# Kernel tuning notes

Measured on AMD Instinct MI355X. Metric: run time of the kernel, lower is better.

The kernel has to match this reference:

```python
import jax, jax.numpy as jnp
import numpy as np

N, E, U, R = 50000, 400000, 32, 32
CUTOFF = 5.0


def _xavier(key, shape):
    fan_out, fan_in = shape
    lim = (6.0 / (fan_in + fan_out)) ** 0.5
    return jax.random.uniform(key, shape, jnp.float32, -lim, lim)


def setup_inputs() -> dict:
    key = jax.random.key(0)
    ks = jax.random.split(key, 13)
    X = jax.random.normal(ks[0], (N, 3, 3, U), jnp.float32)
    edge_index = jax.random.randint(ks[1], (2, E), 0, N)
    edge_weight = jax.random.uniform(ks[2], (E,), jnp.float32)
    edge_attr = jax.random.normal(ks[3], (E, R), jnp.float32)
    W1 = _xavier(ks[4], (U, R)); b1 = jnp.zeros((U,), jnp.float32)
    W2 = _xavier(ks[5], (2 * U, U)); b2 = jnp.zeros((2 * U,), jnp.float32)
    W3 = _xavier(ks[6], (3 * U, 2 * U)); b3 = jnp.zeros((3 * U,), jnp.float32)
    Wt = jnp.stack([_xavier(ks[7 + i], (U, U)) for i in range(6)])  # 6 bias-free tensor linears
    return dict(X=X, edge_index=edge_index, edge_weight=edge_weight, edge_attr=edge_attr,
                W1=W1, b1=b1, W2=W2, b2=b2, W3=W3, b3=b3, Wt=Wt)


def _decompose(T):
    # T: (n, 3, 3, u) -> scalar (full eye*trace/3), skew-symmetric, traceless symmetric parts
    Tt = jnp.swapaxes(T, 1, 2)
    trace = jnp.einsum('niiu->nu', T)
    eye = jnp.eye(3, dtype=T.dtype)[None, :, :, None]
    I = (trace / 3.0)[:, None, None, :] * eye
    A = 0.5 * (T - Tt)
    S = 0.5 * (T + Tt) - I
    return I, A, S


def _lin(T, W):
    # torch nn.Linear (no bias): y = x @ W.T over the trailing units axis
    return jnp.einsum('nijk,mk->nijm', T, W)


def reference(X, edge_index, edge_weight, edge_attr, W1, b1, W2, b2, W3, b3, Wt):
    num_nodes = X.shape[0]
    u = X.shape[-1]
    # cosine cutoff
    Cc = jnp.where(edge_weight < CUTOFF,
                   0.5 * (jnp.cos(edge_weight * jnp.pi / CUTOFF) + 1.0), 0.0)
    # scalar edge MLP
    ea = jax.nn.silu(edge_attr @ W1.T + b1)
    ea = jax.nn.silu(ea @ W2.T + b2)
    ea = jax.nn.silu(ea @ W3.T + b3)
    ea = (ea * Cc[:, None]).reshape(-1, u, 3)  # (E, units, 3)
    # normalize node tensors
    normX = jnp.sum(X ** 2, axis=(1, 2)) + 1.0  # (n, u)
    Xn = X / normX[:, None, None, :]
    # decompose + per-component linears
    I, A, S = _decompose(Xn)
    I = _lin(I, Wt[0]); A = _lin(A, Wt[1]); S = _lin(S, Wt[2])
    Y = I + A + S
    # message passing: gather at dst, weight, scatter-add back to dst
    dst = edge_index[1]
    eaI = ea[..., 0][:, None, None, :]
    eaA = ea[..., 1][:, None, None, :]
    eaS = ea[..., 2][:, None, None, :]
    Im = jax.ops.segment_sum(I[dst] * eaI, dst, num_segments=num_nodes)
    Am = jax.ops.segment_sum(A[dst] * eaA, dst, num_segments=num_nodes)
    Sm = jax.ops.segment_sum(S[dst] * eaS, dst, num_segments=num_nodes)
    msg = Im + Am + Sm
    # O(3) tensor product: Y @ msg + msg @ Y (per node, per unit)
    M = jnp.einsum('nijk,njlk->nilk', Y, msg) + jnp.einsum('nijk,njlk->nilk', msg, Y)
    I, A, S = _decompose(M)
    Xc = I + A + S
    normp1 = (jnp.sum(Xc ** 2, axis=(1, 2)) + 1.0)[:, None, None, :]
    I, A, S = I / normp1, A / normp1, S / normp1
    I = _lin(I, Wt[3]); A = _lin(A, Wt[4]); S = _lin(S, Wt[5])
    dX = I + A + S
    return Xn + dX + jnp.einsum('nijk,njlk->nilk', dX, dX)
```

## Files before the change

kernel.cpp:

```cpp
#include <hip/hip_runtime.h>
#include <math.h>


typedef _Float16 h2    __attribute__((ext_vector_type(2)));
typedef __fp16   p2    __attribute__((ext_vector_type(2)));
typedef _Float16 f16x8 __attribute__((ext_vector_type(8)));
typedef float    f32x4 __attribute__((ext_vector_type(4)));

union U8 { unsigned u[4]; uint4 q; f16x8 v; };
union C4 { float4 f; f32x4 v; };

__device__ __forceinline__ h2 as_h2(unsigned u){ union{unsigned x; h2 h;} c; c.x=u; return c.h; }
__device__ __forceinline__ unsigned h2bits(h2 h){ union{h2 h; unsigned x;} c; c.h=h; return c.x; }

__device__ __forceinline__ float dot2(h2 a, h2 b, float c){
#if __has_builtin(__builtin_amdgcn_fdot2)
    return __builtin_amdgcn_fdot2(a, b, c, false);
#else
    return c + (float)a.x*(float)b.x + (float)a.y*(float)b.y;
#endif
}

__device__ __forceinline__ h2 pk(float a, float b){
#if __has_builtin(__builtin_amdgcn_cvt_pkrtz)
    union { p2 p; h2 h; } c;
    c.p = __builtin_amdgcn_cvt_pkrtz(a, b);
    return c.h;
#else
    h2 r; r.x=(_Float16)a; r.y=(_Float16)b; return r;
#endif
}

__device__ __forceinline__ unsigned pk_rtn(float a, float b){
    union { h2 h; unsigned x; } c;
    c.h.x = (_Float16)a; c.h.y = (_Float16)b;
    return c.x;
}

__device__ __forceinline__ float fast_silu(float x){
    return x * __builtin_amdgcn_rcpf(1.0f + __expf(-x));
}

__global__ __launch_bounds__(256) void prep_kernel(
    const float* __restrict__ Wt,
    const float* __restrict__ W1, const float* __restrict__ b1,
    const float* __restrict__ W2, const float* __restrict__ b2,
    const float* __restrict__ W3, const float* __restrict__ b3,
    unsigned* __restrict__ whn, float* __restrict__ ball, unsigned* __restrict__ wfrag)
{
    int i = blockIdx.x * 256 + threadIdx.x;
    if (i < 4096) {
        int call = i >> 11, r = i & 2047, kp = r >> 7, rem = r & 127;
        int u = rem >> 2, c = rem & 3;
        unsigned val = 0;
        if (c < 3) {
            const float* W = Wt + (size_t)(3*call + c)*1024 + u*32 + 2*kp;
            val = pk_rtn(W[0], W[1]);
        }
        whn[i] = val;
    }
    if (i < 192) {
        float v;
        if (i < 32)      v = b1[i];
        else if (i < 96) v = b2[i-32];
        else {
            int o = i - 96;
            v = b3[(o & 31)*3 + (o >> 5)];
        }
        ball[i] = v;
    }
    if (i < 4608) {
        int f = i >> 8, l = (i >> 2) & 63, wi = i & 3;
        int row = l & 15, qq = l >> 4;
        int kb = 8*qq + 2*wi;
        float v0, v1;
        if (f < 2) {
            int m = 16*f + row;
            v0 = W1[m*32 + kb]; v1 = W1[m*32 + kb + 1];
        } else if (f < 6) {
            int m = 16*(f-2) + row;
            v0 = W2[m*32 + kb]; v1 = W2[m*32 + kb + 1];
        } else {
            int idx = f - 6, mt = idx >> 1, kh = idx & 1;
            int mp = 16*mt + row;
            int om = (mp & 31)*3 + (mp >> 5);
            int k  = 32*kh + kb;
            v0 = W3[om*64 + k]; v1 = W3[om*64 + k + 1];
        }
        wfrag[i] = pk_rtn(v0, v1);
    }
}

__global__ __launch_bounds__(256) void hist_kernel(
    const int* __restrict__ edge_index, int* __restrict__ cnt, int nE)
{
    int e = blockIdx.x * 256 + threadIdx.x;
    if (e < nE) atomicAdd(&cnt[edge_index[nE + e]], 1);
}

__global__ __launch_bounds__(1024) void scanA_kernel(
    const int* __restrict__ cnt, int* __restrict__ rowptr,
    int* __restrict__ csum, int nN)
{
    __shared__ int wsum[16];
    __shared__ int wpre[16];
    int tid = threadIdx.x, lane = tid & 63, wid = tid >> 6;
    int i = blockIdx.x * 1024 + tid;
    int orig = (i < nN) ? cnt[i] : 0;
    int v = orig;
    #pragma unroll
    for (int d = 1; d < 64; d <<= 1) { int o = __shfl_up(v, d); if (lane >= d) v += o; }
    if (lane == 63) wsum[wid] = v;
    __syncthreads();
    if (wid == 0) {
        int s = (lane < 16) ? wsum[lane] : 0;
        #pragma unroll
        for (int d = 1; d < 16; d <<= 1) { int o = __shfl_up(s, d); if (lane >= d) s += o; }
        if (lane < 16) wpre[lane] = s;
    }
    __syncthreads();
    int badd = wid ? wpre[wid - 1] : 0;
    if (i < nN) rowptr[i] = badd + v - orig;
    if (tid == 1023) csum[blockIdx.x] = badd + v;
}

__global__ __launch_bounds__(64) void scanB_kernel(
    int* __restrict__ csum, int* __restrict__ rowptr, int nChunks, int nN)
{
    int lane = threadIdx.x;
    int orig = (lane < nChunks) ? csum[lane] : 0;
    int s = orig;
    #pragma unroll
    for (int d = 1; d < 64; d <<= 1) { int o = __shfl_up(s, d); if (lane >= d) s += o; }
    if (lane < nChunks) csum[lane] = s - orig;
    if (lane == 63) rowptr[nN] = s;
}

__global__ __launch_bounds__(1024) void scanC_kernel(
    const int* __restrict__ csum, int* __restrict__ rowptr, int nN)
{
    int i = blockIdx.x * 1024 + threadIdx.x;
    if (i < nN) rowptr[i] += csum[i >> 10];
}

__global__ __launch_bounds__(256, 4) void edge_mfma_kernel(
    const float* __restrict__ edge_attr,
    const float* __restrict__ edge_weight,
    const int* __restrict__ edge_index,
    const int* __restrict__ rowptr,
    int* __restrict__ cursor,
    const unsigned* __restrict__ wfrag,
    const float* __restrict__ ball,
    float* __restrict__ buf, int nE)
{
    __shared__ __align__(16) uint4 swf[1152];
    __shared__ __align__(16) float sball[192];
    int tid = threadIdx.x;
    {
        const uint4* g4 = reinterpret_cast<const uint4*>(wfrag);
        for (int i = tid; i < 1152; i += 256) swf[i] = g4[i];
        if (tid < 192) sball[tid] = ball[tid];
    }
    __syncthreads();

    int lane = tid & 63;
    int wid  = (blockIdx.x << 2) + (tid >> 6);
    int nW   = gridDim.x << 2;
    int T    = (nE + 15) >> 4;

    U8 aw[6];
    #pragma unroll
    for (int f = 0; f < 6; ++f) aw[f].q = swf[f*64 + lane];
    const uint4* w3p = &swf[6*64 + lane];

    int q = lane >> 4, ecol = lane & 15;
    bool hiq = lane >= 32;
    int sl = ecol + ((lane & 16) << 1);
    int sh = sl + 16;

    unsigned* bufu = reinterpret_cast<unsigned*>(buf);

    int tile = wid;
    float4 pA = make_float4(0,0,0,0), pB = pA; float pew = 0.f;
    int pd = 0, prp = 0;
    if (tile < T) {
        int e = tile*16 + ecol; if (e >= nE) e = nE - 1;
        const float* eap = edge_attr + (size_t)e*32 + q*8;
        pA = *reinterpret_cast<const float4*>(eap);
        pB = *reinterpret_cast<const float4*>(eap + 4);
        pew = edge_weight[e];
        if (lane < 16) { pd = edge_index[nE + e]; prp = rowptr[pd]; }
    }

    for (; tile < T; tile += nW) {
        float4 cA = pA, cB = pB; float ew = pew; int d = pd, rp = prp;
        bool ev = (tile*16 + ecol) < nE;

        int slot = 0;
        if (lane < 16 && ev) slot = rp + atomicAdd(&cursor[d], 1);
        int slotAll = __shfl(slot, ecol);

        int nt = tile + nW;
        if (nt < T) {
            int e = nt*16 + ecol; if (e >= nE) e = nE - 1;
            const float* eap = edge_attr + (size_t)e*32 + q*8;
            pA = *reinterpret_cast<const float4*>(eap);
            pB = *reinterpret_cast<const float4*>(eap + 4);
            pew = edge_weight[e];
            if (lane < 16) { pd = edge_index[nE + e]; prp = rowptr[pd]; }
        }

        U8 bea;
        bea.u[0] = h2bits(pk(cA.x, cA.y));
        bea.u[1] = h2bits(pk(cA.z, cA.w));
        bea.u[2] = h2bits(pk(cB.x, cB.y));
        bea.u[3] = h2bits(pk(cB.z, cB.w));

        unsigned w1w[4];
        #pragma unroll
        for (int t = 0; t < 2; ++t) {
            C4 c; c.f = *reinterpret_cast<const float4*>(&sball[16*t + 4*q]);
            f32x4 acc = c.v;
            acc = __builtin_amdgcn_mfma_f32_16x16x32_f16(aw[t].v, bea.v, acc, 0, 0, 0);
            w1w[2*t]   = h2bits(pk(fast_silu(acc[0]), fast_silu(acc[1])));
            w1w[2*t+1] = h2bits(pk(fast_silu(acc[2]), fast_silu(acc[3])));
        }

        U8 bh1;
        {
            unsigned t0 = (unsigned)__shfl((int)w1w[0], sl), t2 = (unsigned)__shfl((int)w1w[2], sl);
            bh1.u[0] = hiq ? t2 : t0;
            unsigned t1 = (unsigned)__shfl((int)w1w[1], sl), t3 = (unsigned)__shfl((int)w1w[3], sl);
            bh1.u[1] = hiq ? t3 : t1;
            t0 = (unsigned)__shfl((int)w1w[0], sh); t2 = (unsigned)__shfl((int)w1w[2], sh);
            bh1.u[2] = hiq ? t2 : t0;
            t1 = (unsigned)__shfl((int)w1w[1], sh); t3 = (unsigned)__shfl((int)w1w[3], sh);
            bh1.u[3] = hiq ? t3 : t1;
        }

        unsigned w2w[8];
        #pragma unroll
        for (int t = 0; t < 4; ++t) {
            C4 c; c.f = *reinterpret_cast<const float4*>(&sball[32 + 16*t + 4*q]);
            f32x4 acc = c.v;
            acc = __builtin_amdgcn_mfma_f32_16x16x32_f16(aw[2+t].v, bh1.v, acc, 0, 0, 0);
            w2w[2*t]   = h2bits(pk(fast_silu(acc[0]), fast_silu(acc[1])));
            w2w[2*t+1] = h2bits(pk(fast_silu(acc[2]), fast_silu(acc[3])));
        }

        U8 b3f[2];
        #pragma unroll
        for (int h = 0; h < 2; ++h) {
            unsigned ta = (unsigned)__shfl((int)w2w[4*h],   sl), tb = (unsigned)__shfl((int)w2w[4*h+2], sl);
            b3f[h].u[0] = hiq ? tb : ta;
            unsigned tc = (unsigned)__shfl((int)w2w[4*h+1], sl), td = (unsigned)__shfl((int)w2w[4*h+3], sl);
            b3f[h].u[1] = hiq ? td : tc;
            ta = (unsigned)__shfl((int)w2w[4*h],   sh); tb = (unsigned)__shfl((int)w2w[4*h+2], sh);
            b3f[h].u[2] = hiq ? tb : ta;
            tc = (unsigned)__shfl((int)w2w[4*h+1], sh); td = (unsigned)__shfl((int)w2w[4*h+3], sh);
            b3f[h].u[3] = hiq ? td : tc;
        }

        float Cc = (ew < 5.0f) ? 0.5f * (__cosf(ew * 0.6283185307179586f) + 1.0f) : 0.0f;

        size_t sb = (size_t)slotAll * 48 + 2*q;
        #pragma unroll
        for (int mt = 0; mt < 6; ++mt) {
            U8 wa, wb;
            wa.q = w3p[(2*mt)*64];
            wb.q = w3p[(2*mt+1)*64];
            C4 c; c.f = *reinterpret_cast<const float4*>(&sball[96 + 16*mt + 4*q]);
            f32x4 acc = c.v;
            acc = __builtin_amdgcn_mfma_f32_16x16x32_f16(wa.v, b3f[0].v, acc, 0, 0, 0);
            acc = __builtin_amdgcn_mfma_f32_16x16x32_f16(wb.v, b3f[1].v, acc, 0, 0, 0);
            unsigned p0 = h2bits(pk(fast_silu(acc[0])*Cc, fast_silu(acc[1])*Cc));
            unsigned p1 = h2bits(pk(fast_silu(acc[2])*Cc, fast_silu(acc[3])*Cc));
            if (ev) *reinterpret_cast<uint2*>(bufu + sb + 8*mt) = make_uint2(p0, p1);
        }
    }
}

__device__ __forceinline__ void comp_linear2(
    const unsigned* __restrict__ sW, const unsigned* __restrict__ cbu,
    int u, int call, float& Il, float* a, float* s)
{
    const uint4* w4 = reinterpret_cast<const uint4*>(sW) + call*512 + u;
    const uint4* c4 = reinterpret_cast<const uint4*>(cbu);
    Il = 0.f; a[0]=a[1]=a[2]=0.f;
    s[0]=s[1]=s[2]=s[3]=s[4]=s[5]=0.f;
    #pragma unroll
    for (int kp2 = 0; kp2 < 8; ++kp2) {
        uint4 r0 = c4[kp2*5+0], r1 = c4[kp2*5+1], r2 = c4[kp2*5+2],
              r3 = c4[kp2*5+3], r4 = c4[kp2*5+4];
        uint4 w0 = w4[(2*kp2)*32], w1 = w4[(2*kp2+1)*32];
        Il   = dot2(as_h2(r0.x), as_h2(w0.x), Il);
        a[0] = dot2(as_h2(r0.y), as_h2(w0.y), a[0]);
        a[1] = dot2(as_h2(r0.z), as_h2(w0.y), a[1]);
        a[2] = dot2(as_h2(r0.w), as_h2(w0.y), a[2]);
        s[0] = dot2(as_h2(r1.x), as_h2(w0.z), s[0]);
        s[1] = dot2(as_h2(r1.y), as_h2(w0.z), s[1]);
        s[2] = dot2(as_h2(r1.z), as_h2(w0.z), s[2]);
        s[3] = dot2(as_h2(r1.w), as_h2(w0.z), s[3]);
        s[4] = dot2(as_h2(r2.x), as_h2(w0.z), s[4]);
        s[5] = dot2(as_h2(r2.y), as_h2(w0.z), s[5]);
        Il   = dot2(as_h2(r2.z), as_h2(w1.x), Il);
        a[0] = dot2(as_h2(r2.w), as_h2(w1.y), a[0]);
        a[1] = dot2(as_h2(r3.x), as_h2(w1.y), a[1]);
        a[2] = dot2(as_h2(r3.y), as_h2(w1.y), a[2]);
        s[0] = dot2(as_h2(r3.z), as_h2(w1.z), s[0]);
        s[1] = dot2(as_h2(r3.w), as_h2(w1.z), s[1]);
        s[2] = dot2(as_h2(r4.x), as_h2(w1.z), s[2]);
        s[3] = dot2(as_h2(r4.y), as_h2(w1.z), s[3]);
        s[4] = dot2(as_h2(r4.z), as_h2(w1.z), s[4]);
        s[5] = dot2(as_h2(r4.w), as_h2(w1.z), s[5]);
    }
}

__device__ __forceinline__ void compose(float Il, const float* a, const float* s, float (&T)[3][3])
{
    T[0][0] =  Il  + s[0]; T[0][1] =  a[0] + s[1]; T[0][2] =  a[1] + s[2];
    T[1][0] = -a[0] + s[1]; T[1][1] =  Il  + s[3]; T[1][2] =  a[2] + s[4];
    T[2][0] = -a[1] + s[2]; T[2][1] = -a[2] + s[4]; T[2][2] =  Il  + s[5];
}

__global__ __launch_bounds__(256) void node_kernel(
    const float* __restrict__ X,
    const unsigned* __restrict__ whn,
    const int* __restrict__ rowptr,
    const float* __restrict__ buf,
    float* __restrict__ out, int nN)
{
    __shared__ __align__(16) unsigned sW[4096];
    __shared__ __align__(16) _Float16 sC[8][320];

    int tid = threadIdx.x;
    {
        const uint4* g4 = reinterpret_cast<const uint4*>(whn);
        uint4* s4 = reinterpret_cast<uint4*>(sW);
        #pragma unroll
        for (int i = 0; i < 4; ++i) s4[tid + 256*i] = g4[tid + 256*i];
    }

    int ln = tid >> 5, u = tid & 31;
    int n  = blockIdx.x * 8 + ln;
    if (n >= nN) n = nN - 1;
    const unsigned* cbu = reinterpret_cast<const unsigned*>(&sC[ln][0]);
    _Float16* cw = &sC[ln][(u >> 1)*20 + (u & 1)];

    int r0 = rowptr[n], r1 = rowptr[n + 1];
    float sIv = 0.f, sAv = 0.f, sSv = 0.f;
    const _Float16* bp = reinterpret_cast<const _Float16*>(buf) + (size_t)r0 * 96 + u;
    for (int i = r0; i < r1; ++i, bp += 96) {
        sIv += (float)bp[0];
        sAv += (float)bp[32];
        sSv += (float)bp[64];
    }

    const float* xp = X + (size_t)n * 288 + u;
    float x[3][3];
    float nrm = 1.0f;
    #pragma unroll
    for (int i = 0; i < 3; ++i)
        #pragma unroll
        for (int j = 0; j < 3; ++j) {
            float v = xp[(i*3 + j) * 32];
            x[i][j] = v; nrm += v * v;
        }
    float inv = 1.0f / nrm;
    #pragma unroll
    for (int i = 0; i < 3; ++i)
        #pragma unroll
        for (int j = 0; j < 3; ++j) x[i][j] *= inv;

    float tI = (x[0][0] + x[1][1] + x[2][2]) * (1.0f/3.0f);
    cw[0]  = (_Float16)tI;
    cw[2]  = (_Float16)(0.5f * (x[0][1] - x[1][0]));
    cw[4]  = (_Float16)(0.5f * (x[0][2] - x[2][0]));
    cw[6]  = (_Float16)(0.5f * (x[1][2] - x[2][1]));
    cw[8]  = (_Float16)(x[0][0] - tI);
    cw[10] = (_Float16)(0.5f * (x[0][1] + x[1][0]));
    cw[12] = (_Float16)(0.5f * (x[0][2] + x[2][0]));
    cw[14] = (_Float16)(x[1][1] - tI);
    cw[16] = (_Float16)(0.5f * (x[1][2] + x[2][1]));
    cw[18] = (_Float16)(x[2][2] - tI);
    __syncthreads();

    float Il, a[3], s[6];
    comp_linear2(sW, cbu, u, 0, Il, a, s);

    float Ym[3][3], Gm[3][3];
    compose(Il, a, s, Ym);
    float am[3] = {a[0]*sAv, a[1]*sAv, a[2]*sAv};
    float sm[6] = {s[0]*sSv, s[1]*sSv, s[2]*sSv, s[3]*sSv, s[4]*sSv, s[5]*sSv};
    compose(Il * sIv, am, sm, Gm);

    float M[3][3]; float np1 = 1.0f;
    #pragma unroll
    for (int i = 0; i < 3; ++i)
        #pragma unroll
        for (int l = 0; l < 3; ++l) {
            float v = 0.f;
            #pragma unroll
            for (int j = 0; j < 3; ++j) v += Ym[i][j]*Gm[j][l] + Gm[i][j]*Ym[j][l];
            M[i][l] = v; np1 += v * v;
        }
    float rinv = 1.0f / np1;
    float tI2 = (M[0][0] + M[1][1] + M[2][2]) * (1.0f/3.0f);

    __builtin_amdgcn_wave_barrier();
    cw[0]  = (_Float16)(tI2 * rinv);
    cw[2]  = (_Float16)(0.5f * (M[0][1] - M[1][0]) * rinv);
    cw[4]  = (_Float16)(0.5f * (M[0][2] - M[2][0]) * rinv);
    cw[6]  = (_Float16)(0.5f * (M[1][2] - M[2][1]) * rinv);
    cw[8]  = (_Float16)((M[0][0] - tI2) * rinv);
    cw[10] = (_Float16)(0.5f * (M[0][1] + M[1][0]) * rinv);
    cw[12] = (_Float16)(0.5f * (M[0][2] + M[2][0]) * rinv);
    cw[14] = (_Float16)((M[1][1] - tI2) * rinv);
    cw[16] = (_Float16)(0.5f * (M[1][2] + M[2][1]) * rinv);
    cw[18] = (_Float16)((M[2][2] - tI2) * rinv);
    __builtin_amdgcn_wave_barrier();

    comp_linear2(sW, cbu, u, 1, Il, a, s);
    float D[3][3];
    compose(Il, a, s, D);

    float* op = out + (size_t)n * 288 + u;
    #pragma unroll
    for (int i = 0; i < 3; ++i)
        #pragma unroll
        for (int l = 0; l < 3; ++l) {
            float v = x[i][l] + D[i][l];
            #pragma unroll
            for (int j = 0; j < 3; ++j) v += D[i][j] * D[j][l];
            op[(i*3 + l) * 32] = v;
        }
}

extern "C" void kernel_launch(void* const* d_in, const int* in_sizes, int n_in,
                              void* d_out, int out_size, void* d_ws, size_t ws_size,
                              hipStream_t stream) {
    const float* X   = (const float*)d_in[0];
    const int*   ei  = (const int*)d_in[1];
    const float* ew  = (const float*)d_in[2];
    const float* ea  = (const float*)d_in[3];
    const float* W1  = (const float*)d_in[4];
    const float* b1  = (const float*)d_in[5];
    const float* W2  = (const float*)d_in[6];
    const float* b2  = (const float*)d_in[7];
    const float* W3  = (const float*)d_in[8];
    const float* b3  = (const float*)d_in[9];
    const float* Wt  = (const float*)d_in[10];

    int nE = in_sizes[2];
    int nN = in_sizes[0] / 288;
    int nChunks = (nN + 1023) / 1024;

    float* ws       = (float*)d_ws;
    unsigned* whn   = (unsigned*)ws;
    float* ball     = ws + 8192;
    unsigned* wfrag = (unsigned*)(ws + 8448);
    float* buf      = ws + 8448 + 4608;
    size_t buf_f    = (size_t)nE * 48;
    int* ib     = (int*)(buf + buf_f);
    int* cntA   = ib;
    int* cursor = ib + nN;
    int* rowptr = ib + 2 * nN;
    int* csum   = ib + 3 * nN + 1;

    prep_kernel<<<36, 256, 0, stream>>>(Wt, W1, b1, W2, b2, W3, b3, whn, ball, wfrag);
    (void)hipMemsetAsync(cntA, 0, (size_t)2 * nN * sizeof(int), stream);
    hist_kernel<<<(nE + 255) / 256, 256, 0, stream>>>(ei, cntA, nE);
    scanA_kernel<<<nChunks, 1024, 0, stream>>>(cntA, rowptr, csum, nN);
    scanB_kernel<<<1, 64, 0, stream>>>(csum, rowptr, nChunks, nN);
    scanC_kernel<<<nChunks, 1024, 0, stream>>>(csum, rowptr, nN);
    edge_mfma_kernel<<<1536, 256, 0, stream>>>(
        ea, ew, ei, rowptr, cursor, wfrag, ball, buf, nE);
    node_kernel<<<(nN + 7) / 8, 256, 0, stream>>>(
        X, whn, rowptr, buf, (float*)d_out, nN);
}
```

Measured before the change: 315.0 us.

## Fuse memset into prep, merge scan passes, reload edge weights from LDS

```diff
diff --git a/kernel.cpp b/kernel.cpp
--- a/kernel.cpp
+++ b/kernel.cpp
@@ -46,9 +46,11 @@
     const float* __restrict__ W1, const float* __restrict__ b1,
     const float* __restrict__ W2, const float* __restrict__ b2,
     const float* __restrict__ W3, const float* __restrict__ b3,
-    unsigned* __restrict__ whn, float* __restrict__ ball, unsigned* __restrict__ wfrag)
+    unsigned* __restrict__ whn, float* __restrict__ ball, unsigned* __restrict__ wfrag,
+    int* __restrict__ cz, int nZ)
 {
     int i = blockIdx.x * 256 + threadIdx.x;
+    if (i < nZ) cz[i] = 0;
     if (i < 4096) {
         int call = i >> 11, r = i & 2047, kp = r >> 7, rem = r & 127;
         int u = rem >> 2, c = rem & 3;
@@ -124,26 +126,29 @@
     if (tid == 1023) csum[blockIdx.x] = badd + v;
 }
 
-__global__ __launch_bounds__(64) void scanB_kernel(
-    int* __restrict__ csum, int* __restrict__ rowptr, int nChunks, int nN)
-{
-    int lane = threadIdx.x;
-    int orig = (lane < nChunks) ? csum[lane] : 0;
-    int s = orig;
-    #pragma unroll
-    for (int d = 1; d < 64; d <<= 1) { int o = __shfl_up(s, d); if (lane >= d) s += o; }
-    if (lane < nChunks) csum[lane] = s - orig;
-    if (lane == 63) rowptr[nN] = s;
-}
-
 __global__ __launch_bounds__(1024) void scanC_kernel(
-    const int* __restrict__ csum, int* __restrict__ rowptr, int nN)
-{
-    int i = blockIdx.x * 1024 + threadIdx.x;
-    if (i < nN) rowptr[i] += csum[i >> 10];
-}
-
-__global__ __launch_bounds__(256, 4) void edge_mfma_kernel(
+    const int* __restrict__ csum, int* __restrict__ rowptr, int nN, int nChunks)
+{
+    __shared__ int sadd[2];
+    int tid = threadIdx.x;
+    if (tid < 64) {
+        int v  = (tid < nChunks) ? csum[tid] : 0;
+        int pv = (tid < (int)blockIdx.x) ? v : 0;
+        int tv = v;
+        #pragma unroll
+        for (int d = 1; d < 64; d <<= 1) {
+            pv += __shfl_xor(pv, d);
+            tv += __shfl_xor(tv, d);
+        }
+        if (tid == 0) { sadd[0] = pv; sadd[1] = tv; }
+    }
+    __syncthreads();
+    int i = blockIdx.x * 1024 + tid;
+    if (i < nN) rowptr[i] += sadd[0];
+    if (i == nN - 1) rowptr[nN] = sadd[1];
+}
+
+__global__ __launch_bounds__(256) void edge_mfma_kernel(
     const float* __restrict__ edge_attr,
     const float* __restrict__ edge_weight,
     const int* __restrict__ edge_index,
@@ -168,15 +173,13 @@
     int nW   = gridDim.x << 2;
     int T    = (nE + 15) >> 4;
 
-    U8 aw[6];
-    #pragma unroll
-    for (int f = 0; f < 6; ++f) aw[f].q = swf[f*64 + lane];
-    const uint4* w3p = &swf[6*64 + lane];
-
     int q = lane >> 4, ecol = lane & 15;
     bool hiq = lane >= 32;
     int sl = ecol + ((lane & 16) << 1);
     int sh = sl + 16;
+
+    const uint4*  wl  = &swf[lane];
+    const float4* bl4 = reinterpret_cast<const float4*>(sball);
 
     unsigned* bufu = reinterpret_cast<unsigned*>(buf);
 
@@ -196,6 +199,9 @@
         float4 cA = pA, cB = pB; float ew = pew; int d = pd, rp = prp;
         bool ev = (tile*16 + ecol) < nE;
 
+        int ob = 0;
+        asm volatile("" : "+v"(ob));
+
         int slot = 0;
         if (lane < 16 && ev) slot = rp + atomicAdd(&cursor[d], 1);
         int slotAll = __shfl(slot, ecol);
@@ -219,9 +225,10 @@
         unsigned w1w[4];
         #pragma unroll
         for (int t = 0; t < 2; ++t) {
-            C4 c; c.f = *reinterpret_cast<const float4*>(&sball[16*t + 4*q]);
+            U8 wf_; wf_.q = wl[t*64 + ob];
+            C4 c; c.f = bl4[4*t + q + ob];
             f32x4 acc = c.v;
-            acc = __builtin_amdgcn_mfma_f32_16x16x32_f16(aw[t].v, bea.v, acc, 0, 0, 0);
+            acc = __builtin_amdgcn_mfma_f32_16x16x32_f16(wf_.v, bea.v, acc, 0, 0, 0);
             w1w[2*t]   = h2bits(pk(fast_silu(acc[0]), fast_silu(acc[1])));
             w1w[2*t+1] = h2bits(pk(fast_silu(acc[2]), fast_silu(acc[3])));
         }
@@ -241,9 +248,10 @@
         unsigned w2w[8];
         #pragma unroll
         for (int t = 0; t < 4; ++t) {
-            C4 c; c.f = *reinterpret_cast<const float4*>(&sball[32 + 16*t + 4*q]);
+            U8 wf_; wf_.q = wl[(2+t)*64 + ob];
+            C4 c; c.f = bl4[8 + 4*t + q + ob];
             f32x4 acc = c.v;
-            acc = __builtin_amdgcn_mfma_f32_16x16x32_f16(aw[2+t].v, bh1.v, acc, 0, 0, 0);
+            acc = __builtin_amdgcn_mfma_f32_16x16x32_f16(wf_.v, bh1.v, acc, 0, 0, 0);
             w2w[2*t]   = h2bits(pk(fast_silu(acc[0]), fast_silu(acc[1])));
             w2w[2*t+1] = h2bits(pk(fast_silu(acc[2]), fast_silu(acc[3])));
         }
@@ -267,9 +275,9 @@
         #pragma unroll
         for (int mt = 0; mt < 6; ++mt) {
             U8 wa, wb;
-            wa.q = w3p[(2*mt)*64];
-            wb.q = w3p[(2*mt+1)*64];
-            C4 c; c.f = *reinterpret_cast<const float4*>(&sball[96 + 16*mt + 4*q]);
+            wa.q = wl[(6+2*mt)*64 + ob];
+            wb.q = wl[(7+2*mt)*64 + ob];
+            C4 c; c.f = bl4[24 + 4*mt + q + ob];
             f32x4 acc = c.v;
             acc = __builtin_amdgcn_mfma_f32_16x16x32_f16(wa.v, b3f[0].v, acc, 0, 0, 0);
             acc = __builtin_amdgcn_mfma_f32_16x16x32_f16(wb.v, b3f[1].v, acc, 0, 0, 0);
@@ -467,12 +475,12 @@
     int* rowptr = ib + 2 * nN;
     int* csum   = ib + 3 * nN + 1;
 
-    prep_kernel<<<36, 256, 0, stream>>>(Wt, W1, b1, W2, b2, W3, b3, whn, ball, wfrag);
-    (void)hipMemsetAsync(cntA, 0, (size_t)2 * nN * sizeof(int), stream);
+    int zBlocks = (2 * nN + 255) / 256;
+    prep_kernel<<<zBlocks, 256, 0, stream>>>(
+        Wt, W1, b1, W2, b2, W3, b3, whn, ball, wfrag, cntA, 2 * nN);
     hist_kernel<<<(nE + 255) / 256, 256, 0, stream>>>(ei, cntA, nE);
     scanA_kernel<<<nChunks, 1024, 0, stream>>>(cntA, rowptr, csum, nN);
-    scanB_kernel<<<1, 64, 0, stream>>>(csum, rowptr, nChunks, nN);
-    scanC_kernel<<<nChunks, 1024, 0, stream>>>(csum, rowptr, nN);
+    scanC_kernel<<<nChunks, 1024, 0, stream>>>(csum, rowptr, nN, nChunks);
     edge_mfma_kernel<<<1536, 256, 0, stream>>>(
         ea, ew, ei, rowptr, cursor, wfrag, ball, buf, nE);
     node_kernel<<<(nN + 7) / 8, 256, 0, stream>>>(
```

Measured after the change: 269.5 us. -14.5%, faster.
